# Optimization experiments

Hardware: AMD Instinct MI355X
Metric: run time of the kernel (lower is better)

## Reference

```python
import jax, jax.numpy as jnp
import numpy as np

TAU = 2.0      # LIF membrane time constant (spikingjelly LIFNode tau=2.0)
V_TH = 1.0     # default spikingjelly threshold
ALPHA = 2.0    # ATan surrogate default alpha

@jax.custom_vjp
def atan_spike(x):
    # Heaviside forward, ATan surrogate backward (spikingjelly surrogate.ATan)
    return (x >= 0.0).astype(x.dtype)

def _spike_fwd(x):
    return atan_spike(x), x

def _spike_bwd(x, g):
    sg = (ALPHA / 2.0) / (1.0 + (jnp.pi / 2.0 * ALPHA * x) ** 2)
    return (g * sg,)

atan_spike.defvjp(_spike_fwd, _spike_bwd)


def setup_inputs() -> dict:
    key = jax.random.key(0)
    ks = jax.random.split(key, 4)
    B, L, C, H, NL, K = 64, 96, 32, 256, 2, 3
    inputs = jax.random.normal(ks[0], (B, L, C), jnp.float32)
    w_enc = jax.random.normal(ks[1], (H, 1, K), jnp.float32) * (1.0 / np.sqrt(K))
    b_enc = jnp.zeros((H,), jnp.float32)
    w_rnn = jax.random.normal(ks[2], (NL, H, H), jnp.float32) * (1.0 / np.sqrt(H))
    b_rnn = jnp.zeros((NL, H), jnp.float32)
    return {"inputs": inputs, "w_enc": w_enc, "b_enc": b_enc,
            "w_rnn": w_rnn, "b_rnn": b_rnn}


def reference(inputs, w_enc, b_enc, w_rnn, b_rnn):
    B, L, C = inputs.shape
    H = w_enc.shape[0]
    NL = w_rnn.shape[0]
    # --- 'conv' spike encoder: per-channel temporal conv -> [B*C, H, L] ---
    x = inputs.transpose(0, 2, 1).reshape(B * C, 1, L)
    h = jax.lax.conv_general_dilated(x, w_enc, (1,), 'SAME',
                                     dimension_numbers=('NCH', 'OIH', 'NCH'))
    h = h + b_enc[None, :, None]
    h = h.transpose(2, 0, 1)  # [L, B*C, H] time-major for scan

    def step(v, x_t):
        s = x_t
        new_v = []
        for l in range(NL):  # fixed small layer loop
            cur = s @ w_rnn[l].T + b_rnn[l]            # Linear
            vl = v[l] + (cur - v[l]) / TAU             # leaky integrate
            s = atan_spike(vl - V_TH)                  # fire (surrogate grad)
            vl = vl * (1.0 - jax.lax.stop_gradient(s)) # hard reset, detach_reset
            new_v.append(vl)
        return tuple(new_v), (s, new_v[-1])

    v0 = tuple(jnp.zeros((B * C, H), inputs.dtype) for _ in range(NL))
    _, (spks, mems) = jax.lax.scan(step, v0, h)
    # spks: [L, B*C, H] -> [B, C*H, L]
    spks = spks.reshape(L, B, C * H).transpose(1, 2, 0)
    return spks.transpose(0, 2, 1), spks[:, :, -1]
```

## Files before the change

kernel.cpp:

```cpp
#include <hip/hip_runtime.h>
#include <hip/hip_bf16.h>
#include <stdint.h>


using floatx4 = __attribute__((ext_vector_type(4))) float;
using intx4   = __attribute__((ext_vector_type(4))) int;

__global__ void prep_kernel(const float* __restrict__ w_enc,
                            const float* __restrict__ b_enc,
                            const float* __restrict__ w_rnn,
                            const float* __restrict__ b_rnn,
                            double* __restrict__ Wd,
                            double* __restrict__ C0d,
                            signed char* __restrict__ Bw8)
{
    const int o = blockIdx.x;
    const int lane = threadIdx.x;
    const float4 w0v = *(const float4*)(w_rnn + (size_t)o * 256 + lane * 4);
    double a0 = 0.0, a1 = 0.0, a2 = 0.0, ab = 0.0;
#pragma unroll
    for (int e = 0; e < 4; ++e) {
        const int i = lane * 4 + e;
        const double wv = (double)(((const float*)&w0v)[e]);
        a0 += wv * (double)w_enc[i * 3 + 0];
        a1 += wv * (double)w_enc[i * 3 + 1];
        a2 += wv * (double)w_enc[i * 3 + 2];
        ab += wv * (double)b_enc[i];
    }
    for (int off = 32; off > 0; off >>= 1) {
        a0 += __shfl_down(a0, off, 64);
        a1 += __shfl_down(a1, off, 64);
        a2 += __shfl_down(a2, off, 64);
        ab += __shfl_down(ab, off, 64);
    }
    if (lane == 0) {
        Wd[o * 3 + 0] = a0;
        Wd[o * 3 + 1] = a1;
        Wd[o * 3 + 2] = a2;
        C0d[o] = ab + (double)b_rnn[o];
    }
    const float4 w1v = *(const float4*)(w_rnn + 65536 + (size_t)o * 256 + lane * 4);
    unsigned int pack[4] = {0u, 0u, 0u, 0u};
#pragma unroll
    for (int e = 0; e < 4; ++e) {
        float f = ((const float*)&w1v)[e];
        int q = __double2int_rn((double)f * 134217728.0);
        int d3 = ((q + 64) & 127) - 64;  q = (q - d3) >> 7;
        int d2 = ((q + 64) & 127) - 64;  q = (q - d2) >> 7;
        int d1 = ((q + 64) & 127) - 64;  q = (q - d1) >> 7;
        int d0 = q;
        pack[0] |= ((unsigned int)(d0 & 0xFF)) << (8 * e);
        pack[1] |= ((unsigned int)(d1 & 0xFF)) << (8 * e);
        pack[2] |= ((unsigned int)(d2 & 0xFF)) << (8 * e);
        pack[3] |= ((unsigned int)(d3 & 0xFF)) << (8 * e);
    }
#pragma unroll
    for (int l = 0; l < 4; ++l)
        *(unsigned int*)(Bw8 + ((size_t)o * 4 + l) * 256 + lane * 4) = pack[l];
}

__global__ void enc_kernel(const float* __restrict__ inputs,
                           const double* __restrict__ Wd,
                           const double* __restrict__ C0d,
                           unsigned char* __restrict__ s0b)
{
    const int n = blockIdx.x;
    const int tidx = threadIdx.x;
    const int b = n >> 5, c = n & 31;
    __shared__ float xr[98];
    if (tidx < 96)       xr[tidx + 1] = inputs[((size_t)b * 96 + tidx) * 32 + c];
    else if (tidx == 96) xr[0]  = 0.0f;
    else if (tidx == 97) xr[97] = 0.0f;
    __syncthreads();
    const double W0 = Wd[tidx * 3], W1 = Wd[tidx * 3 + 1], W2 = Wd[tidx * 3 + 2];
    const double c0 = C0d[tidx];
    const int wid = tidx >> 6, lane = tidx & 63;
    float v = 0.0f;
    for (int t = 0; t < 96; ++t) {
        float cur = (float)((double)xr[t] * W0 + (double)xr[t + 1] * W1 +
                            (double)xr[t + 2] * W2 + c0);
        float vv = v + (cur - v) * 0.5f;
        int sp = (vv - 1.0f) >= 0.0f;
        v = sp ? 0.0f : vv;
        unsigned long long bal = __ballot(sp);
        if ((lane & 15) == 0) {
            const int j = lane >> 4;
            *(unsigned short*)(s0b + ((size_t)t * 2048 + n) * 32 + 8 * j + 2 * wid)
                = (unsigned short)(bal >> (16 * j));
        }
    }
}

__global__ __launch_bounds__(128, 2) void rnn_kernel(
    const unsigned char* __restrict__ s0b,
    const signed char* __restrict__ Bw8,
    const float* __restrict__ b_rnn,
    float* __restrict__ out0,
    float* __restrict__ out1)
{
    const int tid  = threadIdx.x;
    const int wid  = tid >> 6, lane = tid & 63;
    const int m    = lane & 15, g = lane >> 4;
    const int job  = blockIdx.x * 2 + wid;
    const int rt   = job >> 4;
    const int nw   = rt * 16;
    const int o0   = (job & 15) * 16;

    intx4 bfrag[4][4];
#pragma unroll
    for (int l = 0; l < 4; ++l)
#pragma unroll
        for (int c = 0; c < 4; ++c)
            bfrag[l][c] = *(const intx4*)(Bw8 + ((size_t)(o0 + m) * 4 + l) * 256
                                               + c * 64 + g * 16);
    const float4 biasv = *(const float4*)(b_rnn + 256 + o0 + g * 4);

    float* pb = out0 + ((size_t)(nw >> 5) * 96) * 8192
                     + (size_t)((nw & 31) + m) * 256 + o0 + g * 4;

    const unsigned char* mp = s0b + ((size_t)(nw + m)) * 32 + 8 * g;
    uint2 m0 = *(const uint2*)(mp);
    uint2 m1 = *(const uint2*)(mp + 65536);
    uint2 m2 = *(const uint2*)(mp + 2 * 65536);

    floatx4 v = {0.f, 0.f, 0.f, 0.f};

    #define STEP_MFMA(MASK, ACC0, ACC1, ACC2, ACC3)                            \
    do {                                                                       \
        unsigned int hw_[4] = { (MASK).x & 0xFFFFu, (MASK).x >> 16,            \
                                (MASK).y & 0xFFFFu, (MASK).y >> 16 };          \
        _Pragma("unroll")                                                      \
        for (int c = 0; c < 4; ++c) {                                          \
            unsigned int h_ = hw_[c];                                          \
            intx4 a_;                                                          \
            a_.x = (int)(__umul24( h_        & 0xFu, 0x00204081u) & 0x01010101u); \
            a_.y = (int)(__umul24((h_ >> 4)  & 0xFu, 0x00204081u) & 0x01010101u); \
            a_.z = (int)(__umul24((h_ >> 8)  & 0xFu, 0x00204081u) & 0x01010101u); \
            a_.w = (int)(__umul24((h_ >> 12) & 0xFu, 0x00204081u) & 0x01010101u); \
            ACC0 = __builtin_amdgcn_mfma_i32_16x16x64_i8(bfrag[0][c], a_, ACC0, 0, 0, 0); \
            ACC1 = __builtin_amdgcn_mfma_i32_16x16x64_i8(bfrag[1][c], a_, ACC1, 0, 0, 0); \
            ACC2 = __builtin_amdgcn_mfma_i32_16x16x64_i8(bfrag[2][c], a_, ACC2, 0, 0, 0); \
            ACC3 = __builtin_amdgcn_mfma_i32_16x16x64_i8(bfrag[3][c], a_, ACC3, 0, 0, 0); \
        }                                                                      \
    } while (0)

    #define MEMBRANE(ACC0, ACC1, ACC2, ACC3, SV)                               \
    do {                                                                       \
        _Pragma("unroll")                                                      \
        for (int r = 0; r < 4; ++r) {                                          \
            int a01 = (ACC0)[r] * 128 + (ACC1)[r];      \
            int a23 = (ACC2)[r] * 128 + (ACC3)[r];                             \
            float cur = fmaf((float)a01, 0x1p-13f, (float)a23 * 0x1p-27f)      \
                        + ((const float*)&biasv)[r];                           \
            float vv = v[r];                                                   \
            vv = vv + (cur - vv) * 0.5f;                                       \
            float s = ((vv - 1.0f) >= 0.0f) ? 1.0f : 0.0f;                     \
            v[r] = vv * (1.0f - s);                                            \
            (SV)[r] = s;                                                       \
        }                                                                      \
    } while (0)

    for (int t = 0; t < 93; t += 3) {
        uint2 p3 = *(const uint2*)(mp + (size_t)(t + 3) * 65536);
        uint2 p4 = *(const uint2*)(mp + (size_t)(t + 4) * 65536);
        uint2 p5 = *(const uint2*)(mp + (size_t)(t + 5) * 65536);

        intx4 aa0 = {0,0,0,0}, aa1 = {0,0,0,0}, aa2 = {0,0,0,0}, aa3 = {0,0,0,0};
        intx4 ba0 = {0,0,0,0}, ba1 = {0,0,0,0}, ba2 = {0,0,0,0}, ba3 = {0,0,0,0};
        intx4 ca0 = {0,0,0,0}, ca1 = {0,0,0,0}, ca2 = {0,0,0,0}, ca3 = {0,0,0,0};
        STEP_MFMA(m0, aa0, aa1, aa2, aa3);
        STEP_MFMA(m1, ba0, ba1, ba2, ba3);
        STEP_MFMA(m2, ca0, ca1, ca2, ca3);

        floatx4 sva, svb, svc;
        MEMBRANE(aa0, aa1, aa2, aa3, sva);
        *(floatx4*)pb = sva;
        MEMBRANE(ba0, ba1, ba2, ba3, svb);
        *(floatx4*)(pb + 8192) = svb;
        MEMBRANE(ca0, ca1, ca2, ca3, svc);
        *(floatx4*)(pb + 16384) = svc;

        pb += 24576;
        m0 = p3; m1 = p4; m2 = p5;
    }

    {
        intx4 aa0 = {0,0,0,0}, aa1 = {0,0,0,0}, aa2 = {0,0,0,0}, aa3 = {0,0,0,0};
        intx4 ba0 = {0,0,0,0}, ba1 = {0,0,0,0}, ba2 = {0,0,0,0}, ba3 = {0,0,0,0};
        intx4 ca0 = {0,0,0,0}, ca1 = {0,0,0,0}, ca2 = {0,0,0,0}, ca3 = {0,0,0,0};
        STEP_MFMA(m0, aa0, aa1, aa2, aa3);
        STEP_MFMA(m1, ba0, ba1, ba2, ba3);
        STEP_MFMA(m2, ca0, ca1, ca2, ca3);
        floatx4 sva, svb, svc;
        MEMBRANE(aa0, aa1, aa2, aa3, sva);
        *(floatx4*)pb = sva;
        MEMBRANE(ba0, ba1, ba2, ba3, svb);
        *(floatx4*)(pb + 8192) = svb;
        MEMBRANE(ca0, ca1, ca2, ca3, svc);
        *(floatx4*)(pb + 16384) = svc;
        *(floatx4*)(out1 + (size_t)(nw + m) * 256 + o0 + g * 4) = svc;
    }
    #undef STEP_MFMA
    #undef MEMBRANE
}

extern "C" void kernel_launch(void* const* d_in, const int* in_sizes, int n_in,
                              void* d_out, int out_size, void* d_ws, size_t ws_size,
                              hipStream_t stream) {
    const float* inputs = (const float*)d_in[0];
    const float* w_enc  = (const float*)d_in[1];
    const float* b_enc  = (const float*)d_in[2];
    const float* w_rnn  = (const float*)d_in[3];
    const float* b_rnn  = (const float*)d_in[4];

    float* out0 = (float*)d_out;
    float* out1 = out0 + (size_t)64 * 96 * 8192;

    char* ws = (char*)d_ws;
    double*      Wd  = (double*)(ws);
    double*      C0d = (double*)(ws + 6144);
    signed char* Bw8 = (signed char*)(ws + 8192);
    unsigned char* s0b = (unsigned char*)(ws + 270336);

    prep_kernel<<<256, 64, 0, stream>>>(w_enc, b_enc, w_rnn, b_rnn, Wd, C0d, Bw8);
    enc_kernel<<<2048, 256, 0, stream>>>(inputs, Wd, C0d, s0b);
    rnn_kernel<<<1024, 128, 0, stream>>>(s0b, Bw8, b_rnn, out0, out1);
}
```

Baseline: 252.4 us.

## Compute two output column tiles per wave and remap blocks XCD-aware

Each single-wave block now computes 32 output columns (two 16-wide tiles) for a 16-row tile. This reuses each unpacked spike A-fragment across twice as many MFMAs, halving the bit-expansion work per MFMA and the spike-mask loads per output. The block index is remapped so row tiles are grouped per XCD, which should improve L2 locality of the shared spike data. The cost is doubled B-fragment and accumulator registers (launch bounds set to one block of 64), which lowers occupancy and latency hiding.

```diff
diff --git a/kernel.cpp b/kernel.cpp
--- a/kernel.cpp
+++ b/kernel.cpp
@@ -91,41 +91,46 @@
     }
 }
 
-__global__ __launch_bounds__(128, 2) void rnn_kernel(
+__global__ __launch_bounds__(64, 1) void rnn_kernel(
     const unsigned char* __restrict__ s0b,
     const signed char* __restrict__ Bw8,
     const float* __restrict__ b_rnn,
     float* __restrict__ out0,
     float* __restrict__ out1)
 {
-    const int tid  = threadIdx.x;
-    const int wid  = tid >> 6, lane = tid & 63;
+    const int lane = threadIdx.x & 63;
     const int m    = lane & 15, g = lane >> 4;
-    const int job  = blockIdx.x * 2 + wid;
-    const int rt   = job >> 4;
-    const int nw   = rt * 16;
-    const int o0   = (job & 15) * 16;
-
-    intx4 bfrag[4][4];
-#pragma unroll
-    for (int l = 0; l < 4; ++l)
-#pragma unroll
-        for (int c = 0; c < 4; ++c)
-            bfrag[l][c] = *(const intx4*)(Bw8 + ((size_t)(o0 + m) * 4 + l) * 256
-                                               + c * 64 + g * 16);
-    const float4 biasv = *(const float4*)(b_rnn + 256 + o0 + g * 4);
+
+    const int bidx  = blockIdx.x;
+    const int xcd   = bidx & 7;
+    const int u     = bidx >> 3;
+    const int rt    = 16 * xcd + (u & 15);
+    const int cpair = u >> 4;
+    const int nw    = rt * 16;
+    const int o0    = cpair * 32;
+
+    intx4 bfrag[2][4][4];
+#pragma unroll
+    for (int d = 0; d < 2; ++d)
+#pragma unroll
+        for (int l = 0; l < 4; ++l)
+#pragma unroll
+            for (int c = 0; c < 4; ++c)
+                bfrag[d][l][c] = *(const intx4*)(Bw8
+                    + ((size_t)(o0 + 16 * d + m) * 4 + l) * 256 + c * 64 + g * 16);
+
+    const float4 bias0 = *(const float4*)(b_rnn + 256 + o0 + g * 4);
+    const float4 bias1 = *(const float4*)(b_rnn + 256 + o0 + 16 + g * 4);
 
     float* pb = out0 + ((size_t)(nw >> 5) * 96) * 8192
                      + (size_t)((nw & 31) + m) * 256 + o0 + g * 4;
 
     const unsigned char* mp = s0b + ((size_t)(nw + m)) * 32 + 8 * g;
-    uint2 m0 = *(const uint2*)(mp);
-    uint2 m1 = *(const uint2*)(mp + 65536);
-    uint2 m2 = *(const uint2*)(mp + 2 * 65536);
-
-    floatx4 v = {0.f, 0.f, 0.f, 0.f};
-
-    #define STEP_MFMA(MASK, ACC0, ACC1, ACC2, ACC3)                            \
+
+    floatx4 v0 = {0.f, 0.f, 0.f, 0.f};
+    floatx4 v1 = {0.f, 0.f, 0.f, 0.f};
+
+    #define STEP_MFMA2(MASK, P0, P1, P2, P3, Q0, Q1, Q2, Q3)                   \
     do {                                                                       \
         unsigned int hw_[4] = { (MASK).x & 0xFFFFu, (MASK).x >> 16,            \
                                 (MASK).y & 0xFFFFu, (MASK).y >> 16 };          \
@@ -137,71 +142,96 @@
             a_.y = (int)(__umul24((h_ >> 4)  & 0xFu, 0x00204081u) & 0x01010101u); \
             a_.z = (int)(__umul24((h_ >> 8)  & 0xFu, 0x00204081u) & 0x01010101u); \
             a_.w = (int)(__umul24((h_ >> 12) & 0xFu, 0x00204081u) & 0x01010101u); \
-            ACC0 = __builtin_amdgcn_mfma_i32_16x16x64_i8(bfrag[0][c], a_, ACC0, 0, 0, 0); \
-            ACC1 = __builtin_amdgcn_mfma_i32_16x16x64_i8(bfrag[1][c], a_, ACC1, 0, 0, 0); \
-            ACC2 = __builtin_amdgcn_mfma_i32_16x16x64_i8(bfrag[2][c], a_, ACC2, 0, 0, 0); \
-            ACC3 = __builtin_amdgcn_mfma_i32_16x16x64_i8(bfrag[3][c], a_, ACC3, 0, 0, 0); \
+            P0 = __builtin_amdgcn_mfma_i32_16x16x64_i8(bfrag[0][0][c], a_, P0, 0, 0, 0); \
+            P1 = __builtin_amdgcn_mfma_i32_16x16x64_i8(bfrag[0][1][c], a_, P1, 0, 0, 0); \
+            P2 = __builtin_amdgcn_mfma_i32_16x16x64_i8(bfrag[0][2][c], a_, P2, 0, 0, 0); \
+            P3 = __builtin_amdgcn_mfma_i32_16x16x64_i8(bfrag[0][3][c], a_, P3, 0, 0, 0); \
+            Q0 = __builtin_amdgcn_mfma_i32_16x16x64_i8(bfrag[1][0][c], a_, Q0, 0, 0, 0); \
+            Q1 = __builtin_amdgcn_mfma_i32_16x16x64_i8(bfrag[1][1][c], a_, Q1, 0, 0, 0); \
+            Q2 = __builtin_amdgcn_mfma_i32_16x16x64_i8(bfrag[1][2][c], a_, Q2, 0, 0, 0); \
+            Q3 = __builtin_amdgcn_mfma_i32_16x16x64_i8(bfrag[1][3][c], a_, Q3, 0, 0, 0); \
         }                                                                      \
     } while (0)
 
-    #define MEMBRANE(ACC0, ACC1, ACC2, ACC3, SV)                               \
+    #define MEMBRANE(ACC0, ACC1, ACC2, ACC3, VV, BIAS, SV)                     \
     do {                                                                       \
         _Pragma("unroll")                                                      \
         for (int r = 0; r < 4; ++r) {                                          \
             int a01 = (ACC0)[r] * 128 + (ACC1)[r];      \
             int a23 = (ACC2)[r] * 128 + (ACC3)[r];                             \
             float cur = fmaf((float)a01, 0x1p-13f, (float)a23 * 0x1p-27f)      \
-                        + ((const float*)&biasv)[r];                           \
-            float vv = v[r];                                                   \
+                        + ((const float*)&(BIAS))[r];                          \
+            float vv = (VV)[r];                                                \
             vv = vv + (cur - vv) * 0.5f;                                       \
             float s = ((vv - 1.0f) >= 0.0f) ? 1.0f : 0.0f;                     \
-            v[r] = vv * (1.0f - s);                                            \
+            (VV)[r] = vv * (1.0f - s);                                         \
             (SV)[r] = s;                                                       \
         }                                                                      \
     } while (0)
+
+    #define FINISH_STEP(P0, P1, P2, P3, Q0, Q1, Q2, Q3, PBOFF)                 \
+    do {                                                                       \
+        floatx4 sv0_, sv1_;                                                    \
+        MEMBRANE(P0, P1, P2, P3, v0, bias0, sv0_);                             \
+        *(floatx4*)(pb + (PBOFF)) = sv0_;                                      \
+        MEMBRANE(Q0, Q1, Q2, Q3, v1, bias1, sv1_);                             \
+        *(floatx4*)(pb + (PBOFF) + 16) = sv1_;                                 \
+    } while (0)
+
+    uint2 m0 = *(const uint2*)(mp);
+    uint2 m1 = *(const uint2*)(mp + 65536);
+    uint2 m2 = *(const uint2*)(mp + 2 * 65536);
 
     for (int t = 0; t < 93; t += 3) {
         uint2 p3 = *(const uint2*)(mp + (size_t)(t + 3) * 65536);
         uint2 p4 = *(const uint2*)(mp + (size_t)(t + 4) * 65536);
         uint2 p5 = *(const uint2*)(mp + (size_t)(t + 5) * 65536);
 
-        intx4 aa0 = {0,0,0,0}, aa1 = {0,0,0,0}, aa2 = {0,0,0,0}, aa3 = {0,0,0,0};
-        intx4 ba0 = {0,0,0,0}, ba1 = {0,0,0,0}, ba2 = {0,0,0,0}, ba3 = {0,0,0,0};
-        intx4 ca0 = {0,0,0,0}, ca1 = {0,0,0,0}, ca2 = {0,0,0,0}, ca3 = {0,0,0,0};
-        STEP_MFMA(m0, aa0, aa1, aa2, aa3);
-        STEP_MFMA(m1, ba0, ba1, ba2, ba3);
-        STEP_MFMA(m2, ca0, ca1, ca2, ca3);
-
-        floatx4 sva, svb, svc;
-        MEMBRANE(aa0, aa1, aa2, aa3, sva);
-        *(floatx4*)pb = sva;
-        MEMBRANE(ba0, ba1, ba2, ba3, svb);
-        *(floatx4*)(pb + 8192) = svb;
-        MEMBRANE(ca0, ca1, ca2, ca3, svc);
-        *(floatx4*)(pb + 16384) = svc;
+        intx4 aP0 = {0,0,0,0}, aP1 = {0,0,0,0}, aP2 = {0,0,0,0}, aP3 = {0,0,0,0};
+        intx4 aQ0 = {0,0,0,0}, aQ1 = {0,0,0,0}, aQ2 = {0,0,0,0}, aQ3 = {0,0,0,0};
+        intx4 bP0 = {0,0,0,0}, bP1 = {0,0,0,0}, bP2 = {0,0,0,0}, bP3 = {0,0,0,0};
+        intx4 bQ0 = {0,0,0,0}, bQ1 = {0,0,0,0}, bQ2 = {0,0,0,0}, bQ3 = {0,0,0,0};
+        intx4 cP0 = {0,0,0,0}, cP1 = {0,0,0,0}, cP2 = {0,0,0,0}, cP3 = {0,0,0,0};
+        intx4 cQ0 = {0,0,0,0}, cQ1 = {0,0,0,0}, cQ2 = {0,0,0,0}, cQ3 = {0,0,0,0};
+        STEP_MFMA2(m0, aP0, aP1, aP2, aP3, aQ0, aQ1, aQ2, aQ3);
+        STEP_MFMA2(m1, bP0, bP1, bP2, bP3, bQ0, bQ1, bQ2, bQ3);
+        STEP_MFMA2(m2, cP0, cP1, cP2, cP3, cQ0, cQ1, cQ2, cQ3);
+
+        FINISH_STEP(aP0, aP1, aP2, aP3, aQ0, aQ1, aQ2, aQ3, 0);
+        FINISH_STEP(bP0, bP1, bP2, bP3, bQ0, bQ1, bQ2, bQ3, 8192);
+        FINISH_STEP(cP0, cP1, cP2, cP3, cQ0, cQ1, cQ2, cQ3, 16384);
 
         pb += 24576;
         m0 = p3; m1 = p4; m2 = p5;
     }
 
     {
-        intx4 aa0 = {0,0,0,0}, aa1 = {0,0,0,0}, aa2 = {0,0,0,0}, aa3 = {0,0,0,0};
-        intx4 ba0 = {0,0,0,0}, ba1 = {0,0,0,0}, ba2 = {0,0,0,0}, ba3 = {0,0,0,0};
-        intx4 ca0 = {0,0,0,0}, ca1 = {0,0,0,0}, ca2 = {0,0,0,0}, ca3 = {0,0,0,0};
-        STEP_MFMA(m0, aa0, aa1, aa2, aa3);
-        STEP_MFMA(m1, ba0, ba1, ba2, ba3);
-        STEP_MFMA(m2, ca0, ca1, ca2, ca3);
-        floatx4 sva, svb, svc;
-        MEMBRANE(aa0, aa1, aa2, aa3, sva);
-        *(floatx4*)pb = sva;
-        MEMBRANE(ba0, ba1, ba2, ba3, svb);
-        *(floatx4*)(pb + 8192) = svb;
-        MEMBRANE(ca0, ca1, ca2, ca3, svc);
-        *(floatx4*)(pb + 16384) = svc;
-        *(floatx4*)(out1 + (size_t)(nw + m) * 256 + o0 + g * 4) = svc;
-    }
-    #undef STEP_MFMA
+        intx4 aP0 = {0,0,0,0}, aP1 = {0,0,0,0}, aP2 = {0,0,0,0}, aP3 = {0,0,0,0};
+        intx4 aQ0 = {0,0,0,0}, aQ1 = {0,0,0,0}, aQ2 = {0,0,0,0}, aQ3 = {0,0,0,0};
+        intx4 bP0 = {0,0,0,0}, bP1 = {0,0,0,0}, bP2 = {0,0,0,0}, bP3 = {0,0,0,0};
+        intx4 bQ0 = {0,0,0,0}, bQ1 = {0,0,0,0}, bQ2 = {0,0,0,0}, bQ3 = {0,0,0,0};
+        intx4 cP0 = {0,0,0,0}, cP1 = {0,0,0,0}, cP2 = {0,0,0,0}, cP3 = {0,0,0,0};
+        intx4 cQ0 = {0,0,0,0}, cQ1 = {0,0,0,0}, cQ2 = {0,0,0,0}, cQ3 = {0,0,0,0};
+        STEP_MFMA2(m0, aP0, aP1, aP2, aP3, aQ0, aQ1, aQ2, aQ3);
+        STEP_MFMA2(m1, bP0, bP1, bP2, bP3, bQ0, bQ1, bQ2, bQ3);
+        STEP_MFMA2(m2, cP0, cP1, cP2, cP3, cQ0, cQ1, cQ2, cQ3);
+
+        FINISH_STEP(aP0, aP1, aP2, aP3, aQ0, aQ1, aQ2, aQ3, 0);
+        FINISH_STEP(bP0, bP1, bP2, bP3, bQ0, bQ1, bQ2, bQ3, 8192);
+
+        floatx4 sv0_, sv1_;
+        MEMBRANE(cP0, cP1, cP2, cP3, v0, bias0, sv0_);
+        *(floatx4*)(pb + 16384) = sv0_;
+        MEMBRANE(cQ0, cQ1, cQ2, cQ3, v1, bias1, sv1_);
+        *(floatx4*)(pb + 16384 + 16) = sv1_;
+
+        float* p1 = out1 + (size_t)(nw + m) * 256 + o0 + g * 4;
+        *(floatx4*)p1        = sv0_;
+        *(floatx4*)(p1 + 16) = sv1_;
+    }
+    #undef STEP_MFMA2
     #undef MEMBRANE
+    #undef FINISH_STEP
 }
 
 extern "C" void kernel_launch(void* const* d_in, const int* in_sizes, int n_in,
@@ -224,5 +254,5 @@
 
     prep_kernel<<<256, 64, 0, stream>>>(w_enc, b_enc, w_rnn, b_rnn, Wd, C0d, Bw8);
     enc_kernel<<<2048, 256, 0, stream>>>(inputs, Wd, C0d, s0b);
-    rnn_kernel<<<1024, 128, 0, stream>>>(s0b, Bw8, b_rnn, out0, out1);
-}
+    rnn_kernel<<<1024, 64, 0, stream>>>(s0b, Bw8, b_rnn, out0, out1);
+}
```

Result: no change. 251.3 us (-0.5%).
